# Kernel optimization log

Hardware: AMD Instinct MI355X
Metric: run time of the kernel (lower is better)

Reference implementation:

```python
import jax, jax.numpy as jnp
import numpy as np

D, NH, NL, NP, DFF = 256, 8, 4, 4, 1024
DH = D // NH
SHAPES = [(64, 64), (32, 32), (16, 16), (8, 8)]
LEN = sum(h * w for h, w in SHAPES)  # 5440
B = 4
EPS = 1e-5


def setup_inputs() -> dict:
    key = jax.random.key(0)
    ks = jax.random.split(key, 24)
    def lin_w(k, fin, fout, scale=None):
        s = (1.0 / np.sqrt(fin)) if scale is None else scale
        return jax.random.normal(k, (fin, fout), jnp.float32) * s
    def lin_b(k, fout, scale=0.01):
        return jax.random.normal(k, (fout,), jnp.float32) * scale
    inp = {
        'src': jax.random.normal(ks[0], (B, LEN, D), jnp.float32),
        'pos_lvl_embed': jax.random.normal(ks[1], (B, LEN, D), jnp.float32),
        'spatial_shapes': jnp.array(SHAPES, jnp.int32),
        'level_start_index': jnp.array(np.cumsum([0] + [h * w for h, w in SHAPES[:-1]]), jnp.int32),
        # MSDeformAttn params
        'Wv': lin_w(ks[2], D, D), 'bv': lin_b(ks[3], D),
        'Woff': lin_w(ks[4], D, NH * NL * NP * 2, scale=0.001),  # small offsets, like grid init
        'boff': jax.random.normal(ks[5], (NH * NL * NP * 2,), jnp.float32) * 0.5,
        'Wa': lin_w(ks[6], D, NH * NL * NP), 'ba': lin_b(ks[7], NH * NL * NP),
        'Wo': lin_w(ks[8], D, D), 'bo': lin_b(ks[9], D),
        # FFN params
        'W1': lin_w(ks[10], D, DFF), 'b1': lin_b(ks[11], DFF),
        'W2': lin_w(ks[12], DFF, D), 'b2': lin_b(ks[13], D),
        # LayerNorms
        'g1': jnp.ones((D,), jnp.float32), 'be1': jnp.zeros((D,), jnp.float32),
        'g2': jnp.ones((D,), jnp.float32), 'be2': jnp.zeros((D,), jnp.float32),
    }
    return inp


def _layernorm(x, g, b):
    mu = jnp.mean(x, axis=-1, keepdims=True)
    var = jnp.var(x, axis=-1, keepdims=True)
    return (x - mu) * jax.lax.rsqrt(var + EPS) * g + b


def _bilinear(v, x, y):
    # v: [B, H, W, NH, DH]; x, y: [B, Lq, NH, NP] pixel coords (align_corners=False, zero padding)
    Bv, H, W = v.shape[0], v.shape[1], v.shape[2]
    x0, y0 = jnp.floor(x), jnp.floor(y)
    bb = jnp.arange(Bv)[:, None, None, None]
    hh = jnp.arange(NH)[None, None, :, None]
    out = 0.0
    for dx in (0, 1):
        for dy in (0, 1):
            xi, yi = x0 + dx, y0 + dy
            w = (1.0 - jnp.abs(x - xi)) * (1.0 - jnp.abs(y - yi))
            valid = (xi >= 0) & (xi <= W - 1) & (yi >= 0) & (yi <= H - 1)
            xc = jnp.clip(xi, 0, W - 1).astype(jnp.int32)
            yc = jnp.clip(yi, 0, H - 1).astype(jnp.int32)
            out = out + v[bb, yc, xc, hh] * (w * valid)[..., None]
    return out  # [B, Lq, NH, NP, DH]


def _ms_deform_attn(query, value_flat, shapes, starts, Wv, bv, Woff, boff, Wa, ba, Wo, bo):
    Bq, Lq = query.shape[0], query.shape[1]
    # reference points: normalized center of each query's own spatial location (valid_ratios == 1)
    refs = []
    for (H, W) in shapes:
        gy, gx = jnp.meshgrid(jnp.arange(H, dtype=jnp.float32), jnp.arange(W, dtype=jnp.float32), indexing='ij')
        refs.append(jnp.stack([(gx + 0.5) / W, (gy + 0.5) / H], -1).reshape(-1, 2))
    ref = jnp.concatenate(refs, 0)  # [Len, 2] (x, y)

    value = (value_flat @ Wv + bv).reshape(Bq, Lq, NH, DH)
    off = (query @ Woff + boff).reshape(Bq, Lq, NH, NL, NP, 2)
    attn = jax.nn.softmax((query @ Wa + ba).reshape(Bq, Lq, NH, NL * NP), axis=-1).reshape(Bq, Lq, NH, NL, NP)
    norm = jnp.array([[w, h] for (h, w) in shapes], jnp.float32)  # [NL, 2] = (W, H)
    loc = ref[None, :, None, None, None, :] + off / norm[None, None, None, :, None, :]  # [B,Lq,NH,NL,NP,2]

    out = 0.0
    for l, (H, W) in enumerate(shapes):
        s = starts[l]
        v_l = value[:, s:s + H * W].reshape(Bq, H, W, NH, DH)
        x = loc[:, :, :, l, :, 0] * W - 0.5
        y = loc[:, :, :, l, :, 1] * H - 0.5
        sampled = _bilinear(v_l, x, y)  # [B,Lq,NH,NP,DH]
        out = out + jnp.sum(sampled * attn[:, :, :, l, :, None], axis=3)
    return out.reshape(Bq, Lq, D) @ Wo + bo


def reference(src, spatial_shapes, level_start_index, pos_lvl_embed,
              Wv, bv, Woff, boff, Wa, ba, Wo, bo,
              W1, b1, W2, b2, g1, be1, g2, be2):
    shapes = [(int(h), int(w)) for h, w in np.asarray(spatial_shapes)]  # static metadata
    starts = [int(s) for s in np.asarray(level_start_index)]
    src2 = _ms_deform_attn(src + pos_lvl_embed, src, shapes, starts, Wv, bv, Woff, boff, Wa, ba, Wo, bo)
    x = _layernorm(src + src2, g1, be1)
    ffn = jax.nn.relu(x @ W1 + b1) @ W2 + b2
    return _layernorm(x + ffn, g2, be2)
```

## Files before the change

kernel.cpp:

```cpp
#include <hip/hip_runtime.h>
#include <hip/hip_fp16.h>
#include <cstddef>
#include <cstdint>

#define DMODEL 256
#define NHEAD  8
#define NLVL   4
#define NPT    4
#define DHEAD  32
#define DFFN   1024
#define SLEN   5440
#define BATCH  4
#define NTOK   (BATCH * SLEN)
#define NT256  ((size_t)NTOK * 256)
#define GYR    170
#define GYP    176
#define LN_EPS 1e-5f

typedef __attribute__((ext_vector_type(4))) float f32x4;
typedef __attribute__((ext_vector_type(8))) short s16x8;

__device__ __forceinline__ unsigned short f2bf(float f) {
    union { float f; unsigned u; } v; v.f = f;
    unsigned u = v.u;
    u += 0x7FFFu + ((u >> 16) & 1u);
    return (unsigned short)(u >> 16);
}
__device__ __forceinline__ float bf2f(unsigned short h) {
    union { unsigned u; float f; } v; v.u = ((unsigned)h) << 16;
    return v.f;
}

__device__ __forceinline__ void g2l16(const unsigned short* g, unsigned short* l) {
    __builtin_amdgcn_global_load_lds(
        (const __attribute__((address_space(1))) unsigned int*)g,
        (__attribute__((address_space(3))) unsigned int*)l, 16, 0, 0);
}

__global__ __launch_bounds__(256) void prep_tr_kernel(
    const float* __restrict__ src, const float* __restrict__ pos,
    unsigned short* __restrict__ srcB, unsigned short* __restrict__ qB,
    const float* __restrict__ Wv, const float* __restrict__ Woff,
    const float* __restrict__ Wa, const float* __restrict__ Wo,
    const float* __restrict__ W1, const float* __restrict__ W2,
    unsigned short* __restrict__ WvT, unsigned short* __restrict__ WcatT,
    unsigned short* __restrict__ WoT,
    unsigned short* __restrict__ W1T, unsigned short* __restrict__ W2T)
{
    if (blockIdx.x < 5440) {
        const size_t i = ((size_t)blockIdx.x * 256 + threadIdx.x) * 4;
        const float4 s = *(const float4*)(src + i);
        const float4 p = *(const float4*)(pos + i);
        ushort4 sb, qb;
        sb.x = f2bf(s.x); sb.y = f2bf(s.y); sb.z = f2bf(s.z); sb.w = f2bf(s.w);
        qb.x = f2bf(s.x + p.x); qb.y = f2bf(s.y + p.y);
        qb.z = f2bf(s.z + p.z); qb.w = f2bf(s.w + p.w);
        *(ushort4*)(srcB + i) = sb;
        *(ushort4*)(qB + i) = qb;
        return;
    }
    const int bid = blockIdx.x - 5440;
    const float* W; unsigned short* Wt; int K, N, t;
    if (bid < 16)       { W = Wv;   Wt = WvT;              K = 256;  N = 256;  t = bid; }
    else if (bid < 32)  { W = Woff; Wt = WcatT;            K = 256;  N = 256;  t = bid - 16; }
    else if (bid < 40)  { W = Wa;   Wt = WcatT + 256*256;  K = 256;  N = 128;  t = bid - 32; }
    else if (bid < 56)  { W = Wo;   Wt = WoT;              K = 256;  N = 256;  t = bid - 40; }
    else if (bid < 120) { W = W1;   Wt = W1T;              K = 256;  N = 1024; t = bid - 56; }
    else                { W = W2;   Wt = W2T;              K = 1024; N = 256;  t = bid - 120; }
    const int ntx = N >> 6;
    const int k0 = (t / ntx) * 64, n0 = (t % ntx) * 64;

    __shared__ float T[64][65];
    const int r  = threadIdx.x >> 4;
    const int c4 = (threadIdx.x & 15) * 4;
    #pragma unroll
    for (int rep = 0; rep < 4; rep++) {
        const int k = rep * 16 + r;
        const float4 v = *(const float4*)(W + (size_t)(k0 + k) * N + n0 + c4);
        T[c4 + 0][k] = v.x; T[c4 + 1][k] = v.y;
        T[c4 + 2][k] = v.z; T[c4 + 3][k] = v.w;
    }
    __syncthreads();
    #pragma unroll
    for (int rep = 0; rep < 4; rep++) {
        const int n = rep * 16 + r;
        ushort4 o;
        o.x = f2bf(T[n][c4 + 0]); o.y = f2bf(T[n][c4 + 1]);
        o.z = f2bf(T[n][c4 + 2]); o.w = f2bf(T[n][c4 + 3]);
        *(ushort4*)(Wt + (size_t)(n0 + n) * K + k0 + c4) = o;
    }
}

template <int KK, int NXB, bool RELU, int OM>
__global__ __launch_bounds__(256, 2) void gemm_lds_kernel(
    const unsigned short* __restrict__ A,
    const unsigned short* __restrict__ Bt,
    const float* __restrict__ bias, const float* __restrict__ bias2,
    int bsplit,
    void* __restrict__ Cout, int N)
{
    const int lin = blockIdx.x;
    const int c8  = lin & 7;
    const int rr  = lin >> 3;
    const int bx  = rr % NXB;
    const int yy  = (rr / NXB) * 8 + c8;
    if (yy >= GYR) return;
    const int row0 = yy * 128;
    const int col0 = bx * 128;

    __shared__ __align__(16) unsigned short sA[2][128 * 64];
    __shared__ __align__(16) unsigned short sB[2][128 * 64];

    const int tid  = threadIdx.x;
    const int wid  = tid >> 6;
    const int lane = tid & 63;
    const int m16  = lane & 15;
    const int q    = lane >> 4;
    const int wr   = (wid >> 1) * 64;
    const int wc   = (wid & 1) * 64;

    const int srow = lane >> 3;
    const int schk = (lane & 7) ^ srow;

    auto stage = [&](int buf, int kt) {
        #pragma unroll
        for (int i = 0; i < 4; i++) {
            const int j = wid * 4 + i;
            const int r = j * 8 + srow;
            g2l16(A  + (size_t)(row0 + r) * KK + kt * 64 + schk * 8,
                  &sA[buf][j * 512]);
            g2l16(Bt + (size_t)(col0 + r) * KK + kt * 64 + schk * 8,
                  &sB[buf][j * 512]);
        }
    };

    f32x4 acc[4][4];
    #pragma unroll
    for (int m = 0; m < 4; m++)
        #pragma unroll
        for (int n = 0; n < 4; n++) acc[m][n] = (f32x4){0.f, 0.f, 0.f, 0.f};

    constexpr int NT = KK / 64;
    stage(0, 0);
    stage(1, 1);

    #pragma unroll 1
    for (int kt = 0; kt < NT; kt++) {
        const int cur = kt & 1;

        if (kt + 1 < NT) asm volatile("s_waitcnt vmcnt(8)" ::: "memory");
        else             asm volatile("s_waitcnt vmcnt(0)" ::: "memory");
        __builtin_amdgcn_sched_barrier(0);
        __builtin_amdgcn_s_barrier();
        __builtin_amdgcn_sched_barrier(0);

        #pragma unroll
        for (int ks = 0; ks < 2; ks++) {
            s16x8 a[4], b[4];
            #pragma unroll
            for (int m = 0; m < 4; m++) {
                const int r  = wr + m * 16 + m16;
                const int cc = (ks * 4 + q) ^ (r & 7);
                a[m] = *(const s16x8*)&sA[cur][r * 64 + cc * 8];
            }
            #pragma unroll
            for (int n = 0; n < 4; n++) {
                const int r  = wc + n * 16 + m16;
                const int cc = (ks * 4 + q) ^ (r & 7);
                b[n] = *(const s16x8*)&sB[cur][r * 64 + cc * 8];
            }
            #pragma unroll
            for (int m = 0; m < 4; m++)
                #pragma unroll
                for (int n = 0; n < 4; n++)
                    acc[m][n] = __builtin_amdgcn_mfma_f32_16x16x32_bf16(
                        a[m], b[n], acc[m][n], 0, 0, 0);
        }

        asm volatile("s_waitcnt lgkmcnt(0)" ::: "memory");
        __builtin_amdgcn_sched_barrier(0);
        __builtin_amdgcn_s_barrier();
        __builtin_amdgcn_sched_barrier(0);

        if (kt + 2 < NT) stage(cur, kt + 2);
    }

    #pragma unroll
    for (int n = 0; n < 4; n++) {
        const int col  = col0 + wc + n * 16 + m16;
        const float bc = (col < bsplit) ? bias[col] : bias2[col - bsplit];
        #pragma unroll
        for (int m = 0; m < 4; m++) {
            #pragma unroll
            for (int r = 0; r < 4; r++) {
                const int row = row0 + wr + m * 16 + q * 4 + r;
                float v = acc[m][n][r] + bc;
                if (RELU) v = fmaxf(v, 0.f);
                if (OM == 1)
                    ((unsigned short*)Cout)[(size_t)row * N + col] = f2bf(v);
                else if (OM == 2)
                    ((__half*)Cout)[(size_t)row * N + col] = __float2half(v);
                else
                    ((float*)Cout)[(size_t)row * N + col] = v;
            }
        }
    }
}

__global__ __launch_bounds__(256) void msda_sample_kernel(
    const __half* __restrict__ value, const float* __restrict__ olg,
    unsigned short* __restrict__ out)
{
    const int lin = blockIdx.x;
    const int c8  = lin & 7;
    const int rr  = lin >> 3;
    const int b   = c8 >> 1;
    const int i8  = (c8 & 1) + 2 * rr;

    const int tid = threadIdx.x;
    const int sub = tid & 3;
    const int h   = (tid >> 2) & 7;
    const int t8  = tid >> 5;
    const int q   = i8 * 8 + t8;
    const int bq  = b * SLEN + q;

    __shared__ __align__(16) uint4 smeta[8 * 16 * 8];

    {
        int rem, Wq;
        if (q < 4096)      { rem = q;        Wq = 64; }
        else if (q < 5120) { rem = q - 4096; Wq = 32; }
        else if (q < 5376) { rem = q - 5120; Wq = 16; }
        else               { rem = q - 5376; Wq = 8;  }
        const int gy = rem / Wq;
        const int gx = rem - gy * Wq;
        const float ref_x = (gx + 0.5f) / (float)Wq;
        const float ref_y = (gy + 0.5f) / (float)Wq;

        const float4 lgv = *(const float4*)(olg + (size_t)bq * 384 + 256 + h * 16 + sub * 4);
        float mx = fmaxf(fmaxf(lgv.x, lgv.y), fmaxf(lgv.z, lgv.w));
        mx = fmaxf(mx, __shfl_xor(mx, 1));
        mx = fmaxf(mx, __shfl_xor(mx, 2));
        float e0 = expf(lgv.x - mx), e1 = expf(lgv.y - mx);
        float e2 = expf(lgv.z - mx), e3 = expf(lgv.w - mx);
        float s = e0 + e1 + e2 + e3;
        s += __shfl_xor(s, 1);
        s += __shfl_xor(s, 2);
        const float inv_s = 1.f / s;

        const float4 o01 = *(const float4*)(olg + (size_t)bq * 384 + h * 32 + sub * 8);
        const float4 o23 = *(const float4*)(olg + (size_t)bq * 384 + h * 32 + sub * 8 + 4);

        constexpr int LW[4] = {64, 32, 16, 8};
        constexpr int LS[4] = {0, 4096, 5120, 5376};
        const int Wl = LW[sub];
        const float fW = (float)Wl;
        const float ew[4] = {e0, e1, e2, e3};
        const float ox[4] = {o01.x, o01.z, o23.x, o23.z};
        const float oy[4] = {o01.y, o01.w, o23.y, o23.w};

        #pragma unroll
        for (int j = 0; j < 4; j++) {
            const float aw = ew[j] * inv_s;
            const float X = (ref_x + ox[j] / fW) * fW - 0.5f;
            const float Y = (ref_y + oy[j] / fW) * fW - 0.5f;
            const float x0f = floorf(X), y0f = floorf(Y);
            const float fx = X - x0f, fy = Y - y0f;
            const int x0 = (int)x0f, y0 = (int)y0f;

            unsigned idx[4]; __half hw[4];
            #pragma unroll
            for (int dy = 0; dy < 2; dy++) {
                const int yi = y0 + dy;
                const float wy = dy ? fy : (1.f - fy);
                const bool vy = (yi >= 0) && (yi < Wl);
                const int yc = min(max(yi, 0), Wl - 1);
                #pragma unroll
                for (int dx = 0; dx < 2; dx++) {
                    const int xi = x0 + dx;
                    const float wx = dx ? fx : (1.f - fx);
                    const bool vx = (xi >= 0) && (xi < Wl);
                    const int xc = min(max(xi, 0), Wl - 1);
                    const int c = dy * 2 + dx;
                    idx[c] = (unsigned)(LS[sub] + yc * Wl + xc);
                    hw[c] = __float2half((vx && vy) ? (aw * wx * wy) : 0.f);
                }
            }
            union { __half2 h2; unsigned u; } pk0, pk1;
            pk0.h2 = __halves2half2(hw[0], hw[1]);
            pk1.h2 = __halves2half2(hw[2], hw[3]);
            uint4 m;
            m.x = idx[0] | (idx[1] << 16);
            m.y = idx[2] | (idx[3] << 16);
            m.z = pk0.u;
            m.w = pk1.u;
            smeta[((t8 * 16) + sub * 4 + j) * 8 + h] = m;
        }
    }
    __syncthreads();

    const char* vb = (const char*)value + (size_t)b * SLEN * 512;
    const unsigned laneoff = (unsigned)(h * 64 + sub * 16);
    const uint4* metap = &smeta[(t8 * 16) * 8 + h];

    __half2 acc[4][4];
    #pragma unroll
    for (int i = 0; i < 4; i++)
        #pragma unroll
        for (int k = 0; k < 4; k++)
            acc[i][k] = __float2half2_rn(0.f);

    for (int g = 0; g < 4; g++) {
        #pragma unroll
        for (int pp = 0; pp < 4; pp++) {
            const int p = g * 4 + pp;
            const uint4 m = metap[p * 8];
            const unsigned a0 = ((m.x & 0xFFFFu) << 9) + laneoff;
            const unsigned a1 = ((m.x >> 16) << 9) + laneoff;
            const unsigned a2 = ((m.y & 0xFFFFu) << 9) + laneoff;
            const unsigned a3 = ((m.y >> 16) << 9) + laneoff;
            const int4 v0 = *(const int4*)(vb + a0);
            const int4 v1 = *(const int4*)(vb + a1);
            const int4 v2 = *(const int4*)(vb + a2);
            const int4 v3 = *(const int4*)(vb + a3);
            union { unsigned u; __half2 h2; } wz, ww;
            wz.u = m.z; ww.u = m.w;
            const __half2 ws0 = __half2half2(__low2half(wz.h2));
            const __half2 ws1 = __half2half2(__high2half(wz.h2));
            const __half2 ws2 = __half2half2(__low2half(ww.h2));
            const __half2 ws3 = __half2half2(__high2half(ww.h2));
            const __half2* p0 = (const __half2*)&v0;
            const __half2* p1 = (const __half2*)&v1;
            const __half2* p2 = (const __half2*)&v2;
            const __half2* p3 = (const __half2*)&v3;
            #pragma unroll
            for (int k = 0; k < 4; k++) {
                acc[pp][k] = __hfma2(ws0, p0[k], acc[pp][k]);
                acc[pp][k] = __hfma2(ws1, p1[k], acc[pp][k]);
                acc[pp][k] = __hfma2(ws2, p2[k], acc[pp][k]);
                acc[pp][k] = __hfma2(ws3, p3[k], acc[pp][k]);
            }
        }
    }

    uint4 o;
    unsigned* ou = &o.x;
    #pragma unroll
    for (int k = 0; k < 4; k++) {
        float2 s = {0.f, 0.f};
        #pragma unroll
        for (int i = 0; i < 4; i++) {
            const float2 f = __half22float2(acc[i][k]);
            s.x += f.x; s.y += f.y;
        }
        ou[k] = (unsigned)f2bf(s.x) | ((unsigned)f2bf(s.y) << 16);
    }
    *(uint4*)(out + (size_t)bq * 256 + h * 32 + sub * 8) = o;
}

template <bool X1B, bool X2B, bool WF, bool WB>
__global__ __launch_bounds__(256) void ln_kernel(
    const void* __restrict__ x1, const void* __restrict__ x2,
    const float* __restrict__ g, const float* __restrict__ be,
    float* __restrict__ outf, unsigned short* __restrict__ outb)
{
    const int lane = threadIdx.x & 63;
    const int wid  = threadIdx.x >> 6;
    const size_t row  = (size_t)blockIdx.x * 4 + wid;
    const size_t base = row * 256 + lane * 4;

    float a0, a1, a2, a3, b0, b1, b2, b3;
    if (X1B) {
        const ushort4 a = *(const ushort4*)((const unsigned short*)x1 + base);
        a0 = bf2f(a.x); a1 = bf2f(a.y); a2 = bf2f(a.z); a3 = bf2f(a.w);
    } else {
        const float4 a = *(const float4*)((const float*)x1 + base);
        a0 = a.x; a1 = a.y; a2 = a.z; a3 = a.w;
    }
    if (X2B) {
        const ushort4 b = *(const ushort4*)((const unsigned short*)x2 + base);
        b0 = bf2f(b.x); b1 = bf2f(b.y); b2 = bf2f(b.z); b3 = bf2f(b.w);
    } else {
        const float4 b = *(const float4*)((const float*)x2 + base);
        b0 = b.x; b1 = b.y; b2 = b.z; b3 = b.w;
    }
    const float v0 = a0 + b0, v1 = a1 + b1, v2 = a2 + b2, v3 = a3 + b3;

    float s  = v0 + v1 + v2 + v3;
    float s2 = v0 * v0 + v1 * v1 + v2 * v2 + v3 * v3;
    #pragma unroll
    for (int o = 32; o > 0; o >>= 1) {
        s  += __shfl_xor(s, o);
        s2 += __shfl_xor(s2, o);
    }
    const float mu  = s * (1.f / 256.f);
    const float var = s2 * (1.f / 256.f) - mu * mu;
    const float r   = rsqrtf(var + LN_EPS);

    const float4 gv = *(const float4*)(g  + lane * 4);
    const float4 bv = *(const float4*)(be + lane * 4);
    float4 o4;
    o4.x = (v0 - mu) * r * gv.x + bv.x;
    o4.y = (v1 - mu) * r * gv.y + bv.y;
    o4.z = (v2 - mu) * r * gv.z + bv.z;
    o4.w = (v3 - mu) * r * gv.w + bv.w;
    if (WF) *(float4*)(outf + base) = o4;
    if (WB) {
        ushort4 ob;
        ob.x = f2bf(o4.x); ob.y = f2bf(o4.y); ob.z = f2bf(o4.z); ob.w = f2bf(o4.w);
        *(ushort4*)(outb + base) = ob;
    }
}

extern "C" void kernel_launch(void* const* d_in, const int* in_sizes, int n_in,
                              void* d_out, int out_size, void* d_ws, size_t ws_size,
                              hipStream_t stream)
{
    const float* src  = (const float*)d_in[0];
    const float* pos  = (const float*)d_in[1];
    const float* Wv   = (const float*)d_in[4];
    const float* bv   = (const float*)d_in[5];
    const float* Woff = (const float*)d_in[6];
    const float* boff = (const float*)d_in[7];
    const float* Wa   = (const float*)d_in[8];
    const float* ba   = (const float*)d_in[9];
    const float* Wo   = (const float*)d_in[10];
    const float* bo   = (const float*)d_in[11];
    const float* W1   = (const float*)d_in[12];
    const float* b1   = (const float*)d_in[13];
    const float* W2   = (const float*)d_in[14];
    const float* b2   = (const float*)d_in[15];
    const float* g1   = (const float*)d_in[16];
    const float* be1  = (const float*)d_in[17];
    const float* g2   = (const float*)d_in[18];
    const float* be2  = (const float*)d_in[19];
    float* out = (float*)d_out;

    char* wsp = (char*)d_ws;
    unsigned short* srcB = (unsigned short*)wsp; wsp += NT256 * 2;
    unsigned short* qB   = (unsigned short*)wsp; wsp += NT256 * 2;
    unsigned short* tbufB = srcB;
    __half*         valB = (__half*)wsp;         wsp += NT256 * 2;
    float*          olg  = (float*)wsp;          wsp += (size_t)NTOK * 384 * 4;
    float*          src2 = olg;
    unsigned short* aoB  = (unsigned short*)wsp; wsp += NT256 * 2;
    unsigned short* xB   = (unsigned short*)wsp; wsp += NT256 * 2;
    unsigned short* h    = (unsigned short*)wsp; wsp += (size_t)NTOK * 1024 * 2;
    unsigned short* WvT  = (unsigned short*)wsp; wsp += 256 * 256 * 2;
    unsigned short* WcatT= (unsigned short*)wsp; wsp += 384 * 256 * 2;
    unsigned short* WoT  = (unsigned short*)wsp; wsp += 256 * 256 * 2;
    unsigned short* W1T  = (unsigned short*)wsp; wsp += 1024 * 256 * 2;
    unsigned short* W2T  = (unsigned short*)wsp; wsp += 256 * 1024 * 2;

    const dim3 blk(256);

    prep_tr_kernel<<<dim3(5624), blk, 0, stream>>>(
        src, pos, srcB, qB, Wv, Woff, Wa, Wo, W1, W2,
        WvT, WcatT, WoT, W1T, W2T);

    gemm_lds_kernel<256, 2, false, 2><<<dim3(2 * GYP), blk, 0, stream>>>(
        srcB, WvT, bv, bv, 1 << 30, valB, 256);
    gemm_lds_kernel<256, 3, false, 0><<<dim3(3 * GYP), blk, 0, stream>>>(
        qB, WcatT, boff, ba, 256, olg, 384);
    msda_sample_kernel<<<dim3(NTOK / 8), blk, 0, stream>>>(valB, olg, aoB);
    gemm_lds_kernel<256, 2, false, 0><<<dim3(2 * GYP), blk, 0, stream>>>(
        aoB, WoT, bo, bo, 1 << 30, src2, 256);
    ln_kernel<false, false, false, true><<<dim3(NTOK / 4), blk, 0, stream>>>(
        src, src2, g1, be1, nullptr, xB);
    gemm_lds_kernel<256, 8, true, 1><<<dim3(8 * GYP), blk, 0, stream>>>(
        xB, W1T, b1, b1, 1 << 30, h, 1024);
    gemm_lds_kernel<1024, 2, false, 1><<<dim3(2 * GYP), blk, 0, stream>>>(
        h, W2T, b2, b2, 1 << 30, tbufB, 256);
    ln_kernel<true, true, true, false><<<dim3(NTOK / 4), blk, 0, stream>>>(
        xB, tbufB, g2, be2, out, nullptr);
}
```

Baseline: 243.0 us.

## Add full-width-N GEMM kernel and use it for value, offset, output and FFN2 projections

Introduces a GEMM kernel where each block computes 128 rows against the full N width (256 or 384). It uses double-buffered LDS staging with explicit waitcnt and barriers. This removes the redundant re-reading of the A tile across multiple N-column blocks. In exchange it launches only 170 single-occupancy blocks, which may leave many CUs idle and reduce latency hiding.

```diff
diff --git a/kernel.cpp b/kernel.cpp
--- a/kernel.cpp
+++ b/kernel.cpp
@@ -88,6 +88,128 @@
         o.x = f2bf(T[n][c4 + 0]); o.y = f2bf(T[n][c4 + 1]);
         o.z = f2bf(T[n][c4 + 2]); o.w = f2bf(T[n][c4 + 3]);
         *(ushort4*)(Wt + (size_t)(n0 + n) * K + k0 + c4) = o;
+    }
+}
+
+template <int KK, int BN, bool RELU, int OM>
+__global__ __launch_bounds__(256, 1) void gemm_wide_kernel(
+    const unsigned short* __restrict__ A,
+    const unsigned short* __restrict__ Bt,
+    const float* __restrict__ bias, const float* __restrict__ bias2,
+    int bsplit,
+    void* __restrict__ Cout)
+{
+    const int row0 = blockIdx.x * 128;
+
+    __shared__ __align__(16) unsigned short sA[2][128 * 64];
+    __shared__ __align__(16) unsigned short sB[2][BN * 64];
+
+    const int tid  = threadIdx.x;
+    const int wid  = tid >> 6;
+    const int lane = tid & 63;
+    const int m16  = lane & 15;
+    const int q    = lane >> 4;
+    const int wr   = (wid >> 1) * 64;
+    const int wc   = (wid & 1) * (BN / 2);
+
+    const int srow = lane >> 3;
+    const int schk = (lane & 7) ^ srow;
+
+    constexpr int AI = 4;
+    constexpr int BI = BN / 32;
+    constexpr int NF = BN / 32;
+
+    auto stage = [&](int buf, int kt) {
+        #pragma unroll
+        for (int i = 0; i < AI; i++) {
+            const int j = wid * AI + i;
+            const int r = j * 8 + srow;
+            g2l16(A + (size_t)(row0 + r) * KK + kt * 64 + schk * 8,
+                  &sA[buf][j * 512]);
+        }
+        #pragma unroll
+        for (int i = 0; i < BI; i++) {
+            const int j = wid * BI + i;
+            const int r = j * 8 + srow;
+            g2l16(Bt + (size_t)r * KK + kt * 64 + schk * 8,
+                  &sB[buf][j * 512]);
+        }
+    };
+
+    f32x4 acc[4][NF];
+    #pragma unroll
+    for (int m = 0; m < 4; m++)
+        #pragma unroll
+        for (int n = 0; n < NF; n++) acc[m][n] = (f32x4){0.f, 0.f, 0.f, 0.f};
+
+    constexpr int NT = KK / 64;
+    stage(0, 0);
+    stage(1, 1);
+
+    #pragma unroll 1
+    for (int kt = 0; kt < NT; kt++) {
+        const int cur = kt & 1;
+
+        if (kt + 1 < NT) {
+            if constexpr (BN == 256) asm volatile("s_waitcnt vmcnt(12)" ::: "memory");
+            else                     asm volatile("s_waitcnt vmcnt(16)" ::: "memory");
+        } else {
+            asm volatile("s_waitcnt vmcnt(0)" ::: "memory");
+        }
+        __builtin_amdgcn_sched_barrier(0);
+        __builtin_amdgcn_s_barrier();
+        __builtin_amdgcn_sched_barrier(0);
+
+        #pragma unroll
+        for (int ks = 0; ks < 2; ks++) {
+            s16x8 a[4], b[NF];
+            #pragma unroll
+            for (int m = 0; m < 4; m++) {
+                const int r  = wr + m * 16 + m16;
+                const int cc = (ks * 4 + q) ^ (r & 7);
+                a[m] = *(const s16x8*)&sA[cur][r * 64 + cc * 8];
+            }
+            #pragma unroll
+            for (int n = 0; n < NF; n++) {
+                const int r  = wc + n * 16 + m16;
+                const int cc = (ks * 4 + q) ^ (r & 7);
+                b[n] = *(const s16x8*)&sB[cur][r * 64 + cc * 8];
+            }
+            #pragma unroll
+            for (int m = 0; m < 4; m++)
+                #pragma unroll
+                for (int n = 0; n < NF; n++)
+                    acc[m][n] = __builtin_amdgcn_mfma_f32_16x16x32_bf16(
+                        a[m], b[n], acc[m][n], 0, 0, 0);
+        }
+
+        asm volatile("s_waitcnt lgkmcnt(0)" ::: "memory");
+        __builtin_amdgcn_sched_barrier(0);
+        __builtin_amdgcn_s_barrier();
+        __builtin_amdgcn_sched_barrier(0);
+
+        if (kt + 2 < NT) stage(cur, kt + 2);
+    }
+
+    #pragma unroll
+    for (int n = 0; n < NF; n++) {
+        const int col  = wc + n * 16 + m16;
+        const float bc = (col < bsplit) ? bias[col] : bias2[col - bsplit];
+        #pragma unroll
+        for (int m = 0; m < 4; m++) {
+            #pragma unroll
+            for (int r = 0; r < 4; r++) {
+                const int row = row0 + wr + m * 16 + q * 4 + r;
+                float v = acc[m][n][r] + bc;
+                if (RELU) v = fmaxf(v, 0.f);
+                if (OM == 1)
+                    ((unsigned short*)Cout)[(size_t)row * BN + col] = f2bf(v);
+                else if (OM == 2)
+                    ((__half*)Cout)[(size_t)row * BN + col] = __float2half(v);
+                else
+                    ((float*)Cout)[(size_t)row * BN + col] = v;
+            }
+        }
     }
 }
 
@@ -458,19 +580,19 @@
         src, pos, srcB, qB, Wv, Woff, Wa, Wo, W1, W2,
         WvT, WcatT, WoT, W1T, W2T);
 
-    gemm_lds_kernel<256, 2, false, 2><<<dim3(2 * GYP), blk, 0, stream>>>(
-        srcB, WvT, bv, bv, 1 << 30, valB, 256);
-    gemm_lds_kernel<256, 3, false, 0><<<dim3(3 * GYP), blk, 0, stream>>>(
-        qB, WcatT, boff, ba, 256, olg, 384);
+    gemm_wide_kernel<256, 256, false, 2><<<dim3(GYR), blk, 0, stream>>>(
+        srcB, WvT, bv, bv, 1 << 30, valB);
+    gemm_wide_kernel<256, 384, false, 0><<<dim3(GYR), blk, 0, stream>>>(
+        qB, WcatT, boff, ba, 256, olg);
     msda_sample_kernel<<<dim3(NTOK / 8), blk, 0, stream>>>(valB, olg, aoB);
-    gemm_lds_kernel<256, 2, false, 0><<<dim3(2 * GYP), blk, 0, stream>>>(
-        aoB, WoT, bo, bo, 1 << 30, src2, 256);
+    gemm_wide_kernel<256, 256, false, 0><<<dim3(GYR), blk, 0, stream>>>(
+        aoB, WoT, bo, bo, 1 << 30, src2);
     ln_kernel<false, false, false, true><<<dim3(NTOK / 4), blk, 0, stream>>>(
         src, src2, g1, be1, nullptr, xB);
     gemm_lds_kernel<256, 8, true, 1><<<dim3(8 * GYP), blk, 0, stream>>>(
         xB, W1T, b1, b1, 1 << 30, h, 1024);
-    gemm_lds_kernel<1024, 2, false, 1><<<dim3(2 * GYP), blk, 0, stream>>>(
-        h, W2T, b2, b2, 1 << 30, tbufB, 256);
+    gemm_wide_kernel<1024, 256, false, 1><<<dim3(GYR), blk, 0, stream>>>(
+        h, W2T, b2, b2, 1 << 30, tbufB);
     ln_kernel<true, true, true, false><<<dim3(NTOK / 4), blk, 0, stream>>>(
         xB, tbufB, g2, be2, out, nullptr);
 }
```

Result: slower. 259.9 us (+6.9%).
